# Optimization experiments

Hardware: AMD Instinct MI355X
Metric: run time of the kernel (lower is better)

## Reference

```python
import jax, jax.numpy as jnp
import numpy as np

B, S1, S2, H, HM = 16, 128, 256, 256, 512  # batch, seq1, seq2, per-token hidden, mlp hidden


def setup_inputs() -> dict:
    k = jax.random.key(0)
    ks = jax.random.split(k, 7)
    query = jax.random.normal(ks[0], (B, S1, H), jnp.float32)
    key = jax.random.normal(ks[1], (B, S2, H), jnp.float32)
    value = jax.random.normal(ks[2], (B, S2, H), jnp.float32)
    q_mask = jax.random.randint(ks[3], (B, S1), 0, 2).astype(jnp.float32)
    k_mask = jax.random.randint(ks[4], (B, S2), 0, 2).astype(jnp.float32)
    s1 = 1.0 / np.sqrt(2 * H)
    W1 = jax.random.uniform(ks[5], (2 * H, HM), jnp.float32, -s1, s1)
    b1 = jnp.zeros((HM,), jnp.float32)
    s2 = 1.0 / np.sqrt(HM)
    W2 = jax.random.uniform(ks[6], (HM, 1), jnp.float32, -s2, s2)
    b2 = jnp.zeros((1,), jnp.float32)
    return {"query": query, "key": key, "value": value, "q_mask": q_mask,
            "k_mask": k_mask, "W1": W1, "b1": b1, "W2": W2, "b2": b2}


def reference(query, key, value, q_mask, k_mask, W1, b1, W2, b2):
    # Factor the first Linear over the concat: cat([q,k]) @ W1 == q @ W1[:H] + k @ W1[H:]
    Hq = query.shape[-1]
    qp = jnp.einsum('bqd,dh->bqh', query, W1[:Hq])      # [B,S1,HM]
    kp = jnp.einsum('bkd,dh->bkh', key, W1[Hq:])        # [B,S2,HM]
    hid = jax.nn.relu(qp[:, :, None, :] + kp[:, None, :, :] + b1)  # [B,S1,S2,HM]
    scores = jnp.einsum('bqkh,h->bqk', hid, W2[:, 0]) + b2[0]       # [B,S1,S2]
    mask = q_mask[:, :, None] * k_mask[:, None, :]                   # [B,S1,S2]
    # masked_fill(-inf).exp() == 0 at masked positions
    A = jnp.where(mask == 0, jnp.zeros((), scores.dtype), jnp.exp(scores))
    A_sum = jnp.clip(jnp.sum(A, axis=-1, keepdims=True), 2e-15, None)
    attn = A / A_sum
    return jnp.einsum('bqk,bkd->bqd', attn, value)  # [B,S1,H]
```

## Files before the change

kernel.cpp:

```cpp
#include <hip/hip_runtime.h>
#include <hip/hip_bf16.h>

#define B_  16
#define S1_ 128
#define S2_ 256
#define H_  256
#define HM_ 512
#define QB  4

typedef _Float16 hf2 __attribute__((ext_vector_type(2)));
typedef _Float16 hf4 __attribute__((ext_vector_type(4)));
typedef _Float16 hf8 __attribute__((ext_vector_type(8)));
typedef float    f32x4 __attribute__((ext_vector_type(4)));

static __device__ inline hf2 u2h(unsigned u) {
    union { unsigned u; hf2 h; } x; x.u = u; return x.h;
}

static __device__ inline float dot2(hf2 a, hf2 b, float c) {
#if __has_builtin(__builtin_amdgcn_fdot2)
    return __builtin_amdgcn_fdot2(a, b, c, false);
#else
    asm("v_dot2_f32_f16 %0, %1, %2, %0" : "+v"(c) : "v"(a), "v"(b));
    return c;
#endif
}

__global__ __launch_bounds__(256) void cvtW_kernel(
    const float* __restrict__ W1, _Float16* __restrict__ Wt)
{
    __shared__ float Ls[32][33];
    const int t  = threadIdx.x;
    const int kt = blockIdx.x & 15, nt = blockIdx.x >> 4;

    {
        const int r = t >> 3, c4 = (t & 7) * 4;
        float4 v = *(const float4*)(W1 + (size_t)(kt * 32 + r) * HM_ + nt * 32 + c4);
        Ls[r][c4 + 0] = v.x; Ls[r][c4 + 1] = v.y;
        Ls[r][c4 + 2] = v.z; Ls[r][c4 + 3] = v.w;
    }
    __syncthreads();
    {
        const int n = t >> 3, k4 = (t & 7) * 4;
        hf4 h = { (_Float16)Ls[k4 + 0][n], (_Float16)Ls[k4 + 1][n],
                  (_Float16)Ls[k4 + 2][n], (_Float16)Ls[k4 + 3][n] };
        *(hf4*)(Wt + (size_t)(nt * 32 + n) * HM_ + kt * 32 + k4) = h;
    }
}

__global__ __launch_bounds__(256) void proj_mfma_kernel(
    const float* __restrict__ query,
    const float* __restrict__ key,
    const _Float16* __restrict__ Wt,
    const float* __restrict__ b1,
    _Float16* __restrict__ QPh,
    _Float16* __restrict__ KPTh)
{
    __shared__ _Float16 Xh[64][264];
    __shared__ _Float16 Wh[64][264];

    const int t   = threadIdx.x;
    const int bid = blockIdx.x;
    const bool modeK = bid >= 256;
    const int lb    = modeK ? bid - 256 : bid;
    const int mtile = lb >> 3, ntile = lb & 7;
    const int m0 = mtile * 64, n0 = ntile * 64;
    const float* X = modeK ? key : query;
    const int kw = modeK ? 256 : 0;

#pragma unroll 2
    for (int i = 0; i < 8; ++i) {
        const int g   = t + i * 256;
        const int row = g >> 5, c8 = (g & 31) * 8;
        float4 xa = *(const float4*)(X + (size_t)(m0 + row) * H_ + c8);
        float4 xb = *(const float4*)(X + (size_t)(m0 + row) * H_ + c8 + 4);
        hf8 xh = { (_Float16)xa.x, (_Float16)xa.y, (_Float16)xa.z, (_Float16)xa.w,
                   (_Float16)xb.x, (_Float16)xb.y, (_Float16)xb.z, (_Float16)xb.w };
        *(hf8*)&Xh[row][c8] = xh;
        uint4 wv = *(const uint4*)(Wt + (size_t)(n0 + row) * HM_ + kw + c8);
        *(uint4*)&Wh[row][c8] = wv;
    }
    __syncthreads();

    const int lane = t & 63, wid = t >> 6;
    const int wr = (wid >> 1) * 32;
    const int wc = (wid & 1) * 32;
    const int fr = lane & 15;
    const int fk = (lane >> 4) * 8;

    f32x4 acc[2][2] = {};

#pragma unroll
    for (int s = 0; s < 8; ++s) {
        const int kb = s * 32 + fk;
        hf8 a0 = *(const hf8*)&Xh[wr + fr][kb];
        hf8 a1 = *(const hf8*)&Xh[wr + 16 + fr][kb];
        hf8 b0 = *(const hf8*)&Wh[wc + fr][kb];
        hf8 b1v = *(const hf8*)&Wh[wc + 16 + fr][kb];
        acc[0][0] = __builtin_amdgcn_mfma_f32_16x16x32_f16(a0, b0,  acc[0][0], 0, 0, 0);
        acc[0][1] = __builtin_amdgcn_mfma_f32_16x16x32_f16(a0, b1v, acc[0][1], 0, 0, 0);
        acc[1][0] = __builtin_amdgcn_mfma_f32_16x16x32_f16(a1, b0,  acc[1][0], 0, 0, 0);
        acc[1][1] = __builtin_amdgcn_mfma_f32_16x16x32_f16(a1, b1v, acc[1][1], 0, 0, 0);
    }

    if (!modeK) {
#pragma unroll
        for (int i = 0; i < 2; ++i)
#pragma unroll
        for (int j = 0; j < 2; ++j) {
            const int n = n0 + wc + j * 16 + fr;
#pragma unroll
            for (int r = 0; r < 4; ++r) {
                const int m = m0 + wr + i * 16 + (lane >> 4) * 4 + r;
                QPh[(size_t)m * HM_ + n] = (_Float16)acc[i][j][r];
            }
        }
    } else {
#pragma unroll
        for (int i = 0; i < 2; ++i)
#pragma unroll
        for (int j = 0; j < 2; ++j) {
            const int n = n0 + wc + j * 16 + fr;
            const float bv = b1[n];
#pragma unroll
            for (int r = 0; r < 4; ++r) {
                const int m    = m0 + wr + i * 16 + (lane >> 4) * 4 + r;
                const int bb   = m >> 8, kloc = m & 255;
                KPTh[(((size_t)bb * 64 + (n >> 3)) * 256 + kloc) * 8 + (n & 7)] =
                    (_Float16)(acc[i][j][r] + bv);
            }
        }
    }
}

__global__ __launch_bounds__(512, 4) void attn_kernel(
    const _Float16* __restrict__ QPh,
    const _Float16* __restrict__ KPTh,
    const float* __restrict__ value,
    const float* __restrict__ q_mask,
    const float* __restrict__ k_mask,
    const float* __restrict__ W2,
    const float* __restrict__ b2,
    float* __restrict__ out)
{
    __shared__ __align__(16) _Float16 qp_h[QB][HM_];
    __shared__ __align__(16) _Float16 w2_h[HM_];
    __shared__ __align__(16) float    Ap[2][QB][S2_];
    __shared__ __align__(16) float4   opart[8][QB][64];
    __shared__ float rA_s[QB];
    __shared__ float qm_s[QB];
    __shared__ float km_s[S2_];

    const int t  = threadIdx.x;
    const int k  = t & 255;
    const int hb = t >> 8;

    const int orig = blockIdx.x + (int)gridDim.x * blockIdx.y;
    const int wg   = (orig & 7) * 64 + (orig >> 3);
    const int q0   = (wg & 31) * QB;
    const int b    = wg >> 5;

    {
        if (t < 256) {
            const uint4* src = (const uint4*)(QPh + (size_t)(b * S1_ + q0) * HM_);
            ((uint4*)&qp_h[0][0])[t] = src[t];
            km_s[t] = k_mask[b * S2_ + t];
        } else if (t < 256 + 128) {
            const int i = t - 256;
            float4 wvv = ((const float4*)W2)[i];
            hf4 hv = { (_Float16)wvv.x, (_Float16)wvv.y,
                       (_Float16)wvv.z, (_Float16)wvv.w };
            *(hf4*)&w2_h[i * 4] = hv;
        } else if (t < 256 + 128 + QB) {
            const int i = t - (256 + 128);
            qm_s[i] = q_mask[b * S1_ + q0 + i];
        }
    }
    __syncthreads();

    float accs[QB] = {0.f, 0.f, 0.f, 0.f};
    const uint4* kp8 = (const uint4*)KPTh + ((size_t)b * 64 + hb * 32) * S2_ + k;

    for (int c = 0; c < 32; ++c) {
        uint4 kvu = kp8[(size_t)c * S2_];
        const int hoff = hb * (HM_ / 2) + c * 8;
        uint4 w4u = *(const uint4*)&w2_h[hoff];
        hf2 kv0 = u2h(kvu.x), kv1 = u2h(kvu.y), kv2 = u2h(kvu.z), kv3 = u2h(kvu.w);
        hf2 wv0 = u2h(w4u.x), wv1 = u2h(w4u.y), wv2 = u2h(w4u.z), wv3 = u2h(w4u.w);
        const hf2 zero = (hf2)(_Float16)0;
#pragma unroll
        for (int q = 0; q < QB; ++q) {
            uint4 qvu = *(const uint4*)&qp_h[q][hoff];
            hf2 s;
            s = __builtin_elementwise_max(u2h(qvu.x) + kv0, zero);
            accs[q] = dot2(s, wv0, accs[q]);
            s = __builtin_elementwise_max(u2h(qvu.y) + kv1, zero);
            accs[q] = dot2(s, wv1, accs[q]);
            s = __builtin_elementwise_max(u2h(qvu.z) + kv2, zero);
            accs[q] = dot2(s, wv2, accs[q]);
            s = __builtin_elementwise_max(u2h(qvu.w) + kv3, zero);
            accs[q] = dot2(s, wv3, accs[q]);
        }
    }
#pragma unroll
    for (int q = 0; q < QB; ++q) Ap[hb][q][k] = accs[q];
    __syncthreads();

    {
        const float b2v = b2[0];
#pragma unroll
        for (int i = 0; i < 2; ++i) {
            const int idx = t + i * 512;
            const int q = idx >> 8, kk = idx & 255;
            float sc = Ap[0][q][kk] + Ap[1][q][kk] + b2v;
            Ap[0][q][kk] = (qm_s[q] * km_s[kk] == 0.f) ? 0.f : __expf(sc);
        }
    }
    __syncthreads();

    if (t < QB * 64) {
        const int q = t >> 6, lane = t & 63;
        float p = Ap[0][q][lane] + Ap[0][q][lane + 64] +
                  Ap[0][q][lane + 128] + Ap[0][q][lane + 192];
#pragma unroll
        for (int m = 32; m >= 1; m >>= 1) p += __shfl_xor(p, m, 64);
        if (lane == 0) rA_s[q] = 1.0f / fmaxf(p, 2e-15f);
    }
    __syncthreads();

    {
        const int w = t >> 6, lane = t & 63;
        const float4* vb = (const float4*)(value + (size_t)b * S2_ * H_)
                           + (size_t)(w * 32) * (H_ / 4) + lane;
        float4 o[QB];
#pragma unroll
        for (int q = 0; q < QB; ++q) o[q] = make_float4(0.f, 0.f, 0.f, 0.f);
#pragma unroll 4
        for (int kk = 0; kk < 32; ++kk) {
            float4 v = vb[(size_t)kk * (H_ / 4)];
#pragma unroll
            for (int q = 0; q < QB; ++q) {
                float a = Ap[0][q][w * 32 + kk];
                o[q].x = fmaf(a, v.x, o[q].x); o[q].y = fmaf(a, v.y, o[q].y);
                o[q].z = fmaf(a, v.z, o[q].z); o[q].w = fmaf(a, v.w, o[q].w);
            }
        }
#pragma unroll
        for (int q = 0; q < QB; ++q) opart[w][q][lane] = o[q];
    }
    __syncthreads();

    if (t < QB * 64) {
        const int q = t >> 6, lane = t & 63;
        float4 s = make_float4(0.f, 0.f, 0.f, 0.f);
#pragma unroll
        for (int w = 0; w < 8; ++w) {
            float4 p = opart[w][q][lane];
            s.x += p.x; s.y += p.y; s.z += p.z; s.w += p.w;
        }
        const float r = rA_s[q];
        s.x *= r; s.y *= r; s.z *= r; s.w *= r;
        *(float4*)(out + (size_t)(b * S1_ + q0 + q) * H_ + lane * 4) = s;
    }
}

extern "C" void kernel_launch(void* const* d_in, const int* in_sizes, int n_in,
                              void* d_out, int out_size, void* d_ws, size_t ws_size,
                              hipStream_t stream) {
    const float* query  = (const float*)d_in[0];
    const float* key    = (const float*)d_in[1];
    const float* value  = (const float*)d_in[2];
    const float* q_mask = (const float*)d_in[3];
    const float* k_mask = (const float*)d_in[4];
    const float* W1     = (const float*)d_in[5];
    const float* b1     = (const float*)d_in[6];
    const float* W2     = (const float*)d_in[7];
    const float* b2     = (const float*)d_in[8];
    float*       out    = (float*)d_out;

    _Float16* QPh  = (_Float16*)d_ws;
    _Float16* KPTh = QPh  + (size_t)B_ * S1_ * HM_;
    _Float16* Wt   = KPTh + (size_t)B_ * S2_ * HM_;

    cvtW_kernel<<<256, 256, 0, stream>>>(W1, Wt);

    proj_mfma_kernel<<<768, 256, 0, stream>>>(query, key, Wt, b1, QPh, KPTh);

    attn_kernel<<<dim3(S1_ / QB, B_), 512, 0, stream>>>(
        QPh, KPTh, value, q_mask, k_mask, W2, b2, out);
}
```

Measured before the change: 42.94 us.

## Fuse W1 conversion into projection, stage coalesced stores, skip masked query rows

Removes the separate W1 transpose/convert kernel: the projection kernel now loads fp32 W1 directly, converts it to fp16 and transposes it into shared memory. Accumulator tiles are staged through a shared-memory union so QP/KP results go out as 16-byte coalesced stores instead of scattered 2-byte stores. The attention kernel skips the score and AV work for query rows whose mask is zero, and prefetches the next KP chunk one iteration ahead. This saves a launch and some memory traffic, at the cost of uncoalesced-ish W reads in every projection block and extra branching in the attention inner loops.

Result: slower. 44.77 us (+4.3%).

```diff
diff --git a/kernel.cpp b/kernel.cpp
--- a/kernel.cpp
+++ b/kernel.cpp
@@ -26,38 +26,24 @@
 #endif
 }
 
-__global__ __launch_bounds__(256) void cvtW_kernel(
-    const float* __restrict__ W1, _Float16* __restrict__ Wt)
-{
-    __shared__ float Ls[32][33];
-    const int t  = threadIdx.x;
-    const int kt = blockIdx.x & 15, nt = blockIdx.x >> 4;
-
-    {
-        const int r = t >> 3, c4 = (t & 7) * 4;
-        float4 v = *(const float4*)(W1 + (size_t)(kt * 32 + r) * HM_ + nt * 32 + c4);
-        Ls[r][c4 + 0] = v.x; Ls[r][c4 + 1] = v.y;
-        Ls[r][c4 + 2] = v.z; Ls[r][c4 + 3] = v.w;
-    }
-    __syncthreads();
-    {
-        const int n = t >> 3, k4 = (t & 7) * 4;
-        hf4 h = { (_Float16)Ls[k4 + 0][n], (_Float16)Ls[k4 + 1][n],
-                  (_Float16)Ls[k4 + 2][n], (_Float16)Ls[k4 + 3][n] };
-        *(hf4*)(Wt + (size_t)(nt * 32 + n) * HM_ + kt * 32 + k4) = h;
-    }
-}
-
-__global__ __launch_bounds__(256) void proj_mfma_kernel(
+struct ProjStage {
+    _Float16 Xh[64][264];
+    _Float16 Wh[64][264];
+};
+union ProjU {
+    ProjStage s;
+    _Float16  Ct[64][72];
+};
+
+__global__ __launch_bounds__(256) void proj_kernel(
     const float* __restrict__ query,
     const float* __restrict__ key,
-    const _Float16* __restrict__ Wt,
+    const float* __restrict__ W1,
     const float* __restrict__ b1,
     _Float16* __restrict__ QPh,
     _Float16* __restrict__ KPTh)
 {
-    __shared__ _Float16 Xh[64][264];
-    __shared__ _Float16 Wh[64][264];
+    __shared__ ProjU u;
 
     const int t   = threadIdx.x;
     const int bid = blockIdx.x;
@@ -66,19 +52,32 @@
     const int mtile = lb >> 3, ntile = lb & 7;
     const int m0 = mtile * 64, n0 = ntile * 64;
     const float* X = modeK ? key : query;
-    const int kw = modeK ? 256 : 0;
+    const float* W = W1 + (modeK ? (size_t)H_ * HM_ : 0);
 
 #pragma unroll 2
     for (int i = 0; i < 8; ++i) {
         const int g   = t + i * 256;
         const int row = g >> 5, c8 = (g & 31) * 8;
-        float4 xa = *(const float4*)(X + (size_t)(m0 + row) * H_ + c8);
-        float4 xb = *(const float4*)(X + (size_t)(m0 + row) * H_ + c8 + 4);
+        const float* xs = X + (size_t)(m0 + row) * H_ + c8;
+        float4 xa = *(const float4*)xs;
+        float4 xb = *(const float4*)(xs + 4);
         hf8 xh = { (_Float16)xa.x, (_Float16)xa.y, (_Float16)xa.z, (_Float16)xa.w,
                    (_Float16)xb.x, (_Float16)xb.y, (_Float16)xb.z, (_Float16)xb.w };
-        *(hf8*)&Xh[row][c8] = xh;
-        uint4 wv = *(const uint4*)(Wt + (size_t)(n0 + row) * HM_ + kw + c8);
-        *(uint4*)&Wh[row][c8] = wv;
+        *(hf8*)&u.s.Xh[row][c8] = xh;
+    }
+#pragma unroll 2
+    for (int p = 0; p < 8; ++p) {
+        const int k2 = p * 32 + (t >> 4) * 2;
+        const int n4 = (t & 15) * 4;
+        float4 wa = *(const float4*)(W + (size_t)k2 * HM_ + n0 + n4);
+        float4 wb = *(const float4*)(W + (size_t)(k2 + 1) * HM_ + n0 + n4);
+        const float* fa = (const float*)&wa;
+        const float* fb = (const float*)&wb;
+#pragma unroll
+        for (int j = 0; j < 4; ++j) {
+            hf2 pr = { (_Float16)fa[j], (_Float16)fb[j] };
+            *(hf2*)&u.s.Wh[n4 + j][k2] = pr;
+        }
     }
     __syncthreads();
 
@@ -93,42 +92,49 @@
 #pragma unroll
     for (int s = 0; s < 8; ++s) {
         const int kb = s * 32 + fk;
-        hf8 a0 = *(const hf8*)&Xh[wr + fr][kb];
-        hf8 a1 = *(const hf8*)&Xh[wr + 16 + fr][kb];
-        hf8 b0 = *(const hf8*)&Wh[wc + fr][kb];
-        hf8 b1v = *(const hf8*)&Wh[wc + 16 + fr][kb];
+        hf8 a0  = *(const hf8*)&u.s.Xh[wr + fr][kb];
+        hf8 a1  = *(const hf8*)&u.s.Xh[wr + 16 + fr][kb];
+        hf8 b0  = *(const hf8*)&u.s.Wh[wc + fr][kb];
+        hf8 b1v = *(const hf8*)&u.s.Wh[wc + 16 + fr][kb];
         acc[0][0] = __builtin_amdgcn_mfma_f32_16x16x32_f16(a0, b0,  acc[0][0], 0, 0, 0);
         acc[0][1] = __builtin_amdgcn_mfma_f32_16x16x32_f16(a0, b1v, acc[0][1], 0, 0, 0);
         acc[1][0] = __builtin_amdgcn_mfma_f32_16x16x32_f16(a1, b0,  acc[1][0], 0, 0, 0);
         acc[1][1] = __builtin_amdgcn_mfma_f32_16x16x32_f16(a1, b1v, acc[1][1], 0, 0, 0);
     }
 
+    __syncthreads();
+
+#pragma unroll
+    for (int i = 0; i < 2; ++i)
+#pragma unroll
+    for (int j = 0; j < 2; ++j) {
+        const int nl = wc + j * 16 + fr;
+        const float bv = modeK ? b1[n0 + nl] : 0.f;
+#pragma unroll
+        for (int r = 0; r < 4; ++r) {
+            const int ml = wr + i * 16 + (lane >> 4) * 4 + r;
+            u.Ct[ml][nl] = (_Float16)(acc[i][j][r] + bv);
+        }
+    }
+    __syncthreads();
+
     if (!modeK) {
 #pragma unroll
-        for (int i = 0; i < 2; ++i)
-#pragma unroll
-        for (int j = 0; j < 2; ++j) {
-            const int n = n0 + wc + j * 16 + fr;
-#pragma unroll
-            for (int r = 0; r < 4; ++r) {
-                const int m = m0 + wr + i * 16 + (lane >> 4) * 4 + r;
-                QPh[(size_t)m * HM_ + n] = (_Float16)acc[i][j][r];
-            }
+        for (int p = 0; p < 2; ++p) {
+            const int idx = t + p * 256;
+            const int row = idx >> 3, c = (idx & 7) * 8;
+            *(uint4*)(QPh + (size_t)(m0 + row) * HM_ + n0 + c) =
+                *(const uint4*)&u.Ct[row][c];
         }
     } else {
-#pragma unroll
-        for (int i = 0; i < 2; ++i)
-#pragma unroll
-        for (int j = 0; j < 2; ++j) {
-            const int n = n0 + wc + j * 16 + fr;
-            const float bv = b1[n];
-#pragma unroll
-            for (int r = 0; r < 4; ++r) {
-                const int m    = m0 + wr + i * 16 + (lane >> 4) * 4 + r;
-                const int bb   = m >> 8, kloc = m & 255;
-                KPTh[(((size_t)bb * 64 + (n >> 3)) * 256 + kloc) * 8 + (n & 7)] =
-                    (_Float16)(acc[i][j][r] + bv);
-            }
+        const int bb = m0 >> 8, kbase = m0 & 255;
+#pragma unroll
+        for (int p = 0; p < 2; ++p) {
+            const int idx = t + p * 256;
+            const int h8l = idx >> 6, kl = idx & 63;
+            const int h8  = (n0 >> 3) + h8l;
+            *(uint4*)(KPTh + (((size_t)bb * 64 + h8) * 256 + kbase + kl) * 8) =
+                *(const uint4*)&u.Ct[kl][h8l * 8];
         }
     }
 }
@@ -160,29 +166,34 @@
     const int q0   = (wg & 31) * QB;
     const int b    = wg >> 5;
 
-    {
-        if (t < 256) {
-            const uint4* src = (const uint4*)(QPh + (size_t)(b * S1_ + q0) * HM_);
-            ((uint4*)&qp_h[0][0])[t] = src[t];
-            km_s[t] = k_mask[b * S2_ + t];
-        } else if (t < 256 + 128) {
-            const int i = t - 256;
-            float4 wvv = ((const float4*)W2)[i];
-            hf4 hv = { (_Float16)wvv.x, (_Float16)wvv.y,
-                       (_Float16)wvv.z, (_Float16)wvv.w };
-            *(hf4*)&w2_h[i * 4] = hv;
-        } else if (t < 256 + 128 + QB) {
-            const int i = t - (256 + 128);
-            qm_s[i] = q_mask[b * S1_ + q0 + i];
-        }
-    }
-    __syncthreads();
+    if (t < 256) {
+        const uint4* src = (const uint4*)(QPh + (size_t)(b * S1_ + q0) * HM_);
+        ((uint4*)&qp_h[0][0])[t] = src[t];
+        km_s[t] = k_mask[b * S2_ + t];
+    } else if (t < 256 + 128) {
+        const int i = t - 256;
+        float4 wvv = ((const float4*)W2)[i];
+        hf4 hv = { (_Float16)wvv.x, (_Float16)wvv.y,
+                   (_Float16)wvv.z, (_Float16)wvv.w };
+        *(hf4*)&w2_h[i * 4] = hv;
+    } else if (t < 256 + 128 + QB) {
+        const int i = t - (256 + 128);
+        qm_s[i] = q_mask[b * S1_ + q0 + i];
+    }
+    __syncthreads();
+
+    const bool qa0 = qm_s[0] != 0.f;
+    const bool qa1 = qm_s[1] != 0.f;
+    const bool qa2 = qm_s[2] != 0.f;
+    const bool qa3 = qm_s[3] != 0.f;
 
     float accs[QB] = {0.f, 0.f, 0.f, 0.f};
     const uint4* kp8 = (const uint4*)KPTh + ((size_t)b * 64 + hb * 32) * S2_ + k;
 
+    uint4 kvu = kp8[0];
     for (int c = 0; c < 32; ++c) {
-        uint4 kvu = kp8[(size_t)c * S2_];
+        uint4 nxt;
+        if (c < 31) nxt = kp8[(size_t)(c + 1) * S2_];
         const int hoff = hb * (HM_ / 2) + c * 8;
         uint4 w4u = *(const uint4*)&w2_h[hoff];
         hf2 kv0 = u2h(kvu.x), kv1 = u2h(kvu.y), kv2 = u2h(kvu.z), kv3 = u2h(kvu.w);
@@ -190,17 +201,21 @@
         const hf2 zero = (hf2)(_Float16)0;
 #pragma unroll
         for (int q = 0; q < QB; ++q) {
-            uint4 qvu = *(const uint4*)&qp_h[q][hoff];
-            hf2 s;
-            s = __builtin_elementwise_max(u2h(qvu.x) + kv0, zero);
-            accs[q] = dot2(s, wv0, accs[q]);
-            s = __builtin_elementwise_max(u2h(qvu.y) + kv1, zero);
-            accs[q] = dot2(s, wv1, accs[q]);
-            s = __builtin_elementwise_max(u2h(qvu.z) + kv2, zero);
-            accs[q] = dot2(s, wv2, accs[q]);
-            s = __builtin_elementwise_max(u2h(qvu.w) + kv3, zero);
-            accs[q] = dot2(s, wv3, accs[q]);
-        }
+            const bool act = (q == 0) ? qa0 : (q == 1) ? qa1 : (q == 2) ? qa2 : qa3;
+            if (act) {
+                uint4 qvu = *(const uint4*)&qp_h[q][hoff];
+                hf2 s;
+                s = __builtin_elementwise_max(u2h(qvu.x) + kv0, zero);
+                accs[q] = dot2(s, wv0, accs[q]);
+                s = __builtin_elementwise_max(u2h(qvu.y) + kv1, zero);
+                accs[q] = dot2(s, wv1, accs[q]);
+                s = __builtin_elementwise_max(u2h(qvu.z) + kv2, zero);
+                accs[q] = dot2(s, wv2, accs[q]);
+                s = __builtin_elementwise_max(u2h(qvu.w) + kv3, zero);
+                accs[q] = dot2(s, wv3, accs[q]);
+            }
+        }
+        kvu = nxt;
     }
 #pragma unroll
     for (int q = 0; q < QB; ++q) Ap[hb][q][k] = accs[q];
@@ -240,9 +255,12 @@
             float4 v = vb[(size_t)kk * (H_ / 4)];
 #pragma unroll
             for (int q = 0; q < QB; ++q) {
-                float a = Ap[0][q][w * 32 + kk];
-                o[q].x = fmaf(a, v.x, o[q].x); o[q].y = fmaf(a, v.y, o[q].y);
-                o[q].z = fmaf(a, v.z, o[q].z); o[q].w = fmaf(a, v.w, o[q].w);
+                const bool act = (q == 0) ? qa0 : (q == 1) ? qa1 : (q == 2) ? qa2 : qa3;
+                if (act) {
+                    float a = Ap[0][q][w * 32 + kk];
+                    o[q].x = fmaf(a, v.x, o[q].x); o[q].y = fmaf(a, v.y, o[q].y);
+                    o[q].z = fmaf(a, v.z, o[q].z); o[q].w = fmaf(a, v.w, o[q].w);
+                }
             }
         }
 #pragma unroll
@@ -279,12 +297,9 @@
     float*       out    = (float*)d_out;
 
     _Float16* QPh  = (_Float16*)d_ws;
-    _Float16* KPTh = QPh  + (size_t)B_ * S1_ * HM_;
-    _Float16* Wt   = KPTh + (size_t)B_ * S2_ * HM_;
-
-    cvtW_kernel<<<256, 256, 0, stream>>>(W1, Wt);
-
-    proj_mfma_kernel<<<768, 256, 0, stream>>>(query, key, Wt, b1, QPh, KPTh);
+    _Float16* KPTh = QPh + (size_t)B_ * S1_ * HM_;
+
+    proj_kernel<<<768, 256, 0, stream>>>(query, key, W1, b1, QPh, KPTh);
 
     attn_kernel<<<dim3(S1_ / QB, B_), 512, 0, stream>>>(
         QPh, KPTh, value, q_mask, k_mask, W2, b2, out);
```
